# Kernel optimization log

Hardware: AMD Instinct MI355X
Metric: run time of the kernel (lower is better)

The kernel has to match this reference:

```python
import jax, jax.numpy as jnp
import numpy as np

NUM_HEADS = 12


def setup_inputs() -> dict:
    key = jax.random.key(0)
    ks = jax.random.split(key, 5)
    B, S, D = 4, 2048, 768
    scale = 0.02
    return {
        "hidden_states": jax.random.normal(ks[0], (B, S, D), dtype=jnp.float32),
        "c_attn_w": jax.random.normal(ks[1], (D, 3 * D), dtype=jnp.float32) * scale,
        "c_attn_b": jax.random.normal(ks[2], (3 * D,), dtype=jnp.float32) * scale,
        "c_proj_w": jax.random.normal(ks[3], (D, D), dtype=jnp.float32) * scale,
        "c_proj_b": jax.random.normal(ks[4], (D,), dtype=jnp.float32) * scale,
    }


def reference(hidden_states, c_attn_w, c_attn_b, c_proj_w, c_proj_b):
    B, S, D = hidden_states.shape
    H = NUM_HEADS
    hd = D // H

    # fused QKV projection (HF Conv1D: x @ W + b, W is [in, out])
    qkv = hidden_states @ c_attn_w + c_attn_b  # [B, S, 3D]
    q, k, v = jnp.split(qkv, 3, axis=-1)

    def split_heads(t):
        return t.reshape(B, S, H, hd).transpose(0, 2, 1, 3)  # [B, H, S, hd]

    q, k, v = split_heads(q), split_heads(k), split_heads(v)

    # scaled dot-product scores (scale_attn_weights=True -> / sqrt(head_dim))
    scores = jnp.einsum("bhqd,bhkd->bhqk", q, k) / jnp.asarray(
        np.sqrt(hd), dtype=q.dtype
    )

    # causal mask: where(tril, scores, dtype_min) as in eager GPT2Attention
    causal = jnp.tril(jnp.ones((S, S), dtype=bool))
    mask_value = jnp.finfo(scores.dtype).min
    scores = jnp.where(causal[None, None, :, :], scores, mask_value)

    attn = jax.nn.softmax(scores, axis=-1)  # attn_dropout p=0 (eval)

    out = jnp.einsum("bhqk,bhkd->bhqd", attn, v)
    out = out.transpose(0, 2, 1, 3).reshape(B, S, D)  # merge heads

    # output projection (resid_dropout p=0)
    return out @ c_proj_w + c_proj_b
```

## Files before the change

kernel.cpp:

```cpp
#include <hip/hip_runtime.h>
#include <stdint.h>

typedef __attribute__((ext_vector_type(8))) short short8;
typedef __attribute__((ext_vector_type(4))) short short4v;
typedef __attribute__((ext_vector_type(8))) __bf16 bf16x8;
typedef __attribute__((ext_vector_type(4))) float f32x4;

#define SEQ 2048
#define DMODEL 768
#define NHEAD 12
#define HD 64
#define NBATCH 4

__device__ __forceinline__ float bf2f(unsigned short u) {
    return __uint_as_float(((unsigned int)u) << 16);
}
__device__ __forceinline__ unsigned short f2bf(float f) {
    unsigned int u = __float_as_uint(f);
    u += 0x7fffu + ((u >> 16) & 1u);
    return (unsigned short)(u >> 16);
}
__device__ __forceinline__ unsigned short f2bfn(float f) {
    union { __bf16 h; unsigned short u; } cv;
    cv.h = (__bf16)f;
    return cv.u;
}
__device__ __forceinline__ short8 cvt8(float4 a, float4 b) {
    short8 r;
    r[0] = (short)f2bf(a.x); r[1] = (short)f2bf(a.y);
    r[2] = (short)f2bf(a.z); r[3] = (short)f2bf(a.w);
    r[4] = (short)f2bf(b.x); r[5] = (short)f2bf(b.y);
    r[6] = (short)f2bf(b.z); r[7] = (short)f2bf(b.w);
    return r;
}
__device__ __forceinline__ f32x4 mfma16(short8 a, short8 b, f32x4 c) {
    return __builtin_amdgcn_mfma_f32_16x16x32_bf16(
        __builtin_bit_cast(bf16x8, a), __builtin_bit_cast(bf16x8, b), c, 0, 0, 0);
}
__device__ __forceinline__ void gload16(const unsigned short* g, unsigned short* l) {
    __builtin_amdgcn_global_load_lds(
        (const __attribute__((address_space(1))) unsigned int*)g,
        (__attribute__((address_space(3))) unsigned int*)l, 16, 0, 0);
}

__global__ void detect_k(const unsigned short* x, const unsigned short* w1,
                         const unsigned short* b1, const unsigned short* w2,
                         const unsigned short* b2, int* flags) {
    const int w = threadIdx.x >> 6, l = threadIdx.x & 63;
    if (w >= 5) return;
    const unsigned short* ptrs[5] = {x, w1, b1, w2, b2};
    const unsigned short* p = ptrs[w];
    float mx = 0.f;
    for (int j = l; j < 1024; j += 64) {
        float v = fabsf(bf2f(p[j]));
        if (!(v <= 1e30f)) v = 1e31f;
        if (v > mx) mx = v;
    }
#pragma unroll
    for (int off = 1; off < 64; off <<= 1) mx = fmaxf(mx, __shfl_xor(mx, off, 64));
    if (l == 0) flags[w] = (mx > 1e3f) ? 1 : 0;
}

__global__ __launch_bounds__(256) void cvt_x(
    const float* __restrict__ Xf, const unsigned short* __restrict__ Xh,
    unsigned short* __restrict__ Xb, const int* __restrict__ flags, int n8) {
    int i = blockIdx.x * 256 + threadIdx.x;
    if (i >= n8) return;
    if (flags[0]) {
        float4 a = ((const float4*)Xf)[(size_t)i * 2];
        float4 b = ((const float4*)Xf)[(size_t)i * 2 + 1];
        *(short8*)&Xb[(size_t)i * 8] = cvt8(a, b);
    } else {
        ((uint4*)Xb)[i] = ((const uint4*)Xh)[i];
    }
}

__global__ __launch_bounds__(256) void convert_wt(
    const float* __restrict__ Wf, const unsigned short* __restrict__ Wh,
    unsigned short* __restrict__ Wt, int R, int C,
    const int* __restrict__ flags, int fidx) {

    __shared__ unsigned short tile[64][65];
    const int c0 = blockIdx.x * 64, r0 = blockIdx.y * 64;
    const int t = threadIdx.x;
    const int ri = t >> 2, cj = (t & 3) * 16;
    const bool f32 = flags[fidx] != 0;

    if (f32) {
#pragma unroll
        for (int u = 0; u < 4; u++) {
            float4 v = *(const float4*)&Wf[(size_t)(r0 + ri) * C + c0 + cj + u * 4];
            tile[ri][cj + u * 4 + 0] = f2bf(v.x);
            tile[ri][cj + u * 4 + 1] = f2bf(v.y);
            tile[ri][cj + u * 4 + 2] = f2bf(v.z);
            tile[ri][cj + u * 4 + 3] = f2bf(v.w);
        }
    } else {
        uint4 a = *(const uint4*)&Wh[(size_t)(r0 + ri) * C + c0 + cj];
        uint4 b = *(const uint4*)&Wh[(size_t)(r0 + ri) * C + c0 + cj + 8];
        *(uint4*)&tile[ri][cj] = a;
        *(uint4*)&tile[ri][cj + 8] = b;
    }
    __syncthreads();

    const int ci = t >> 2, rj = (t & 3) * 16;
    unsigned short tmp[16];
#pragma unroll
    for (int u = 0; u < 16; u++) tmp[u] = tile[rj + u][ci];
    *(uint4*)&Wt[(size_t)(c0 + ci) * R + r0 + rj]     = *(uint4*)&tmp[0];
    *(uint4*)&Wt[(size_t)(c0 + ci) * R + r0 + rj + 8] = *(uint4*)&tmp[8];
}

__global__ __launch_bounds__(256, 3) void gemm_bt(
    const float* __restrict__ Af, const unsigned short* __restrict__ Ah,
    const unsigned short* __restrict__ Bt,
    const float* __restrict__ biasf, const unsigned short* __restrict__ biash,
    int K, int mode, const int* __restrict__ flags, int aFidx, int bFidx,
    unsigned short* __restrict__ out0, unsigned short* __restrict__ out1,
    unsigned short* __restrict__ out2, float* __restrict__ outf) {

    __shared__ __align__(16) unsigned short As[128][32];
    __shared__ __align__(16) unsigned short Bs[128][32];

    const int mBase = blockIdx.y * 128;
    const int nBase = blockIdx.x * 128;
    const int t = threadIdx.x;
    const int w = t >> 6, l = t & 63, lr = l & 15, lk = l >> 4;
    const int wr = w >> 1, wc = w & 1;

    const bool af32 = (aFidx >= 0) && (flags[aFidx] != 0);
    const bool bf32 = flags[bFidx] != 0;

    f32x4 zero = {0.f, 0.f, 0.f, 0.f};
    f32x4 acc[4][4];
#pragma unroll
    for (int i = 0; i < 4; i++)
#pragma unroll
        for (int j = 0; j < 4; j++) acc[i][j] = zero;

    const int arow = t >> 2;
    const int acol = (t & 3) * 8;
    const float* Afp = Af + (size_t)mBase * K;
    const unsigned short* Ahp = Ah + (size_t)mBase * K;
    const unsigned short* Bp = Bt + (size_t)nBase * K;

    const int ch0 = (w * 2 + 0) * 64 + l;
    const int ch1 = (w * 2 + 1) * 64 + l;
    unsigned short* BsF = &Bs[0][0];
    unsigned short* AsF = &As[0][0];

    for (int k0 = 0; k0 < K; k0 += 32) {
        gload16(&Bp[(size_t)(ch0 >> 2) * K + k0 + (ch0 & 3) * 8], BsF + (size_t)(w * 2 + 0) * 512);
        gload16(&Bp[(size_t)(ch1 >> 2) * K + k0 + (ch1 & 3) * 8], BsF + (size_t)(w * 2 + 1) * 512);
        if (af32) {
            float4 f0 = *(const float4*)&Afp[(size_t)arow * K + k0 + acol];
            float4 f1 = *(const float4*)&Afp[(size_t)arow * K + k0 + acol + 4];
            float4 f2 = *(const float4*)&Afp[(size_t)(arow + 64) * K + k0 + acol];
            float4 f3 = *(const float4*)&Afp[(size_t)(arow + 64) * K + k0 + acol + 4];
            *(short8*)&As[arow][acol]      = cvt8(f0, f1);
            *(short8*)&As[arow + 64][acol] = cvt8(f2, f3);
        } else {
            gload16(&Ahp[(size_t)(ch0 >> 2) * K + k0 + (ch0 & 3) * 8], AsF + (size_t)(w * 2 + 0) * 512);
            gload16(&Ahp[(size_t)(ch1 >> 2) * K + k0 + (ch1 & 3) * 8], AsF + (size_t)(w * 2 + 1) * 512);
        }
        __syncthreads();

        short8 a[4], b[4];
#pragma unroll
        for (int i = 0; i < 4; i++)
            a[i] = *(const short8*)&As[wr * 64 + i * 16 + lr][lk * 8];
#pragma unroll
        for (int j = 0; j < 4; j++)
            b[j] = *(const short8*)&Bs[wc * 64 + j * 16 + lr][lk * 8];
#pragma unroll
        for (int i = 0; i < 4; i++)
#pragma unroll
            for (int j = 0; j < 4; j++) acc[i][j] = mfma16(a[i], b[j], acc[i][j]);
        __syncthreads();
    }

#pragma unroll
    for (int j = 0; j < 4; j++) {
        int col = nBase + wc * 64 + j * 16 + lr;
        float bv = bf32 ? biasf[col] : bf2f(biash[col]);
        if (mode == 0 && col >= 1536) {
            int c2 = col - 1536;
            int h = c2 >> 6, d = c2 & 63;
#pragma unroll
            for (int i = 0; i < 4; i++) {
                int row0 = mBase + wr * 64 + i * 16 + lk * 4;
                int bb = row0 >> 11, s0 = row0 & 2047;
                short4v hv4;
#pragma unroll
                for (int r = 0; r < 4; r++) hv4[r] = (short)f2bf(acc[i][j][r] + bv);
                *(short4v*)&out2[(((size_t)(bb * NHEAD + h)) * HD + d) * SEQ + s0] = hv4;
            }
        } else {
#pragma unroll
            for (int i = 0; i < 4; i++) {
                int row0 = mBase + wr * 64 + i * 16 + lk * 4;
#pragma unroll
                for (int r = 0; r < 4; r++) {
                    int row = row0 + r;
                    float fv = acc[i][j][r] + bv;
                    if (mode == 0) {
                        int bb = row >> 11;
                        int s  = row & 2047;
                        unsigned short hv = f2bf(fv);
                        if (col < 768) {
                            int h = col >> 6, d = col & 63;
                            out0[(((size_t)(bb * NHEAD + h)) * SEQ + s) * HD + d] = hv;
                        } else {
                            int c2 = col - 768;
                            int h = c2 >> 6, d = c2 & 63;
                            out1[(((size_t)(bb * NHEAD + h)) * SEQ + s) * HD + d] = hv;
                        }
                    } else {
                        outf[(size_t)row * DMODEL + col] = fv;
                    }
                }
            }
        }
    }
}

__global__ __launch_bounds__(256, 3) void flash_attn(
    const unsigned short* __restrict__ Q, const unsigned short* __restrict__ Km,
    const unsigned short* __restrict__ Vt, unsigned short* __restrict__ Oatt) {

    const int h  = blockIdx.x;
    const int px = blockIdx.y;
    const int b  = blockIdx.z;
    const int bh = b * NHEAD + h;
    const int qtA = 31 - px;
    const int qtB = px;
    const int t = threadIdx.x, w = t >> 6, l = t & 63, lr = l & 15, lk = l >> 4;
    const int qbA = qtA * 64 + w * 16;
    const int qbB = qtB * 64 + w * 16;

    const unsigned short* Qp = Q + (size_t)bh * SEQ * HD;
    const unsigned short* Kp = Km + (size_t)bh * SEQ * HD;
    const unsigned short* Vp = Vt + (size_t)bh * HD * SEQ;

    __shared__ __align__(16) unsigned short Ks[2][4096];
    __shared__ __align__(16) unsigned short Vs[2][4096];
    __shared__ __align__(16) unsigned short Pb[4][2][1024];

    unsigned short* PwA = &Pb[w][0][0];
    unsigned short* PwB = &Pb[w][1][0];

    short8 qA0 = *(const short8*)&Qp[(size_t)(qbA + lr) * HD + lk * 8];
    short8 qA1 = *(const short8*)&Qp[(size_t)(qbA + lr) * HD + 32 + lk * 8];
    short8 qB0 = *(const short8*)&Qp[(size_t)(qbB + lr) * HD + lk * 8];
    short8 qB1 = *(const short8*)&Qp[(size_t)(qbB + lr) * HD + 32 + lk * 8];

    f32x4 zero = {0.f, 0.f, 0.f, 0.f};
    f32x4 oA[4], oB[4];
    float lA[4] = {0.f, 0.f, 0.f, 0.f}, lB[4] = {0.f, 0.f, 0.f, 0.f};
#pragma unroll
    for (int dt = 0; dt < 4; dt++) { oA[dt] = zero; oB[dt] = zero; }

    const float SCL2E = 0.125f * 1.44269504088896f;

#pragma unroll
    for (int q = 0; q < 2; ++q) {
        const int c = w * 128 + q * 64 + l;
        const int row = c >> 3;
        const int ch = (c & 7) ^ (row & 7);
        gload16(&Kp[(size_t)row * HD + ch * 8], &Ks[0][(w * 128 + q * 64) * 8]);
        gload16(&Vp[(size_t)row * SEQ + ch * 8], &Vs[0][(w * 128 + q * 64) * 8]);
    }
    __syncthreads();

    for (int kt = 0; kt <= qtA; ++kt) {
        const int cur = kt & 1;
        if (kt < qtA) {
            const int kn = kt + 1;
#pragma unroll
            for (int q = 0; q < 2; ++q) {
                const int c = w * 128 + q * 64 + l;
                const int row = c >> 3;
                const int ch = (c & 7) ^ (row & 7);
                gload16(&Kp[(size_t)(kn * 64 + row) * HD + ch * 8],
                        &Ks[cur ^ 1][(w * 128 + q * 64) * 8]);
                gload16(&Vp[(size_t)row * SEQ + kn * 64 + ch * 8],
                        &Vs[cur ^ 1][(w * 128 + q * 64) * 8]);
            }
        }
        const bool doB = (kt <= qtB);

        f32x4 s0[4], s1[4];
#pragma unroll
        for (int ct = 0; ct < 4; ct++) { s0[ct] = zero; s1[ct] = zero; }
#pragma unroll
        for (int ct = 0; ct < 4; ct++) {
            const int row = ct * 16 + lr, sw = row & 7;
            short8 k0 = *(const short8*)&Ks[cur][(row * 8 + (lk ^ sw)) * 8];
            short8 k1 = *(const short8*)&Ks[cur][(row * 8 + ((4 | lk) ^ sw)) * 8];
            s0[ct] = mfma16(qA0, k0, s0[ct]);
            s0[ct] = mfma16(qA1, k1, s0[ct]);
            if (doB) {
                s1[ct] = mfma16(qB0, k0, s1[ct]);
                s1[ct] = mfma16(qB1, k1, s1[ct]);
            }
        }

        {
            float p[4][4];
#pragma unroll
            for (int ct = 0; ct < 4; ct++)
#pragma unroll
                for (int r = 0; r < 4; r++) p[ct][r] = s0[ct][r] * SCL2E;
            if (kt == qtA) {
#pragma unroll
                for (int ct = 0; ct < 4; ct++) {
                    const int col = kt * 64 + ct * 16 + lr;
#pragma unroll
                    for (int r = 0; r < 4; r++)
                        if (col > qbA + lk * 4 + r) p[ct][r] = -30000.0f;
                }
            }
#pragma unroll
            for (int ct = 0; ct < 4; ct++)
#pragma unroll
                for (int r = 0; r < 4; r++) p[ct][r] = exp2f(p[ct][r]);
#pragma unroll
            for (int r = 0; r < 4; r++)
                lA[r] += (p[0][r] + p[1][r]) + (p[2][r] + p[3][r]);
#pragma unroll
            for (int ct = 0; ct < 4; ct++) {
                const int pch = ct * 2 + (lr >> 3);
#pragma unroll
                for (int r = 0; r < 4; r++) {
                    const int prow = lk * 4 + r;
                    PwA[(prow * 8 + (pch ^ (prow & 7))) * 8 + (lr & 7)] = f2bfn(p[ct][r]);
                }
            }
        }
        short8 paA0 = *(const short8*)&PwA[(lr * 8 + (lk ^ (lr & 7))) * 8];
        short8 paA1 = *(const short8*)&PwA[(lr * 8 + ((4 | lk) ^ (lr & 7))) * 8];

        short8 paB0 = {0,0,0,0,0,0,0,0}, paB1 = {0,0,0,0,0,0,0,0};
        if (doB) {
            float p[4][4];
#pragma unroll
            for (int ct = 0; ct < 4; ct++)
#pragma unroll
                for (int r = 0; r < 4; r++) p[ct][r] = s1[ct][r] * SCL2E;
            if (kt == qtB) {
#pragma unroll
                for (int ct = 0; ct < 4; ct++) {
                    const int col = kt * 64 + ct * 16 + lr;
#pragma unroll
                    for (int r = 0; r < 4; r++)
                        if (col > qbB + lk * 4 + r) p[ct][r] = -30000.0f;
                }
            }
#pragma unroll
            for (int ct = 0; ct < 4; ct++)
#pragma unroll
                for (int r = 0; r < 4; r++) p[ct][r] = exp2f(p[ct][r]);
#pragma unroll
            for (int r = 0; r < 4; r++)
                lB[r] += (p[0][r] + p[1][r]) + (p[2][r] + p[3][r]);
#pragma unroll
            for (int ct = 0; ct < 4; ct++) {
                const int pch = ct * 2 + (lr >> 3);
#pragma unroll
                for (int r = 0; r < 4; r++) {
                    const int prow = lk * 4 + r;
                    PwB[(prow * 8 + (pch ^ (prow & 7))) * 8 + (lr & 7)] = f2bfn(p[ct][r]);
                }
            }
            paB0 = *(const short8*)&PwB[(lr * 8 + (lk ^ (lr & 7))) * 8];
            paB1 = *(const short8*)&PwB[(lr * 8 + ((4 | lk) ^ (lr & 7))) * 8];
        }

#pragma unroll
        for (int dt = 0; dt < 4; dt++) {
            const int row = dt * 16 + lr, sw = row & 7;
            short8 v0 = *(const short8*)&Vs[cur][(row * 8 + (lk ^ sw)) * 8];
            short8 v1 = *(const short8*)&Vs[cur][(row * 8 + ((4 | lk) ^ sw)) * 8];
            oA[dt] = mfma16(paA0, v0, oA[dt]);
            oA[dt] = mfma16(paA1, v1, oA[dt]);
            if (doB) {
                oB[dt] = mfma16(paB0, v0, oB[dt]);
                oB[dt] = mfma16(paB1, v1, oB[dt]);
            }
        }
        __syncthreads();
    }

#pragma unroll
    for (int r = 0; r < 4; r++) {
#pragma unroll
        for (int off = 1; off < 16; off <<= 1) {
            lA[r] += __shfl_xor(lA[r], off, 64);
            lB[r] += __shfl_xor(lB[r], off, 64);
        }
    }

#pragma unroll
    for (int r = 0; r < 4; r++) {
        const float invA = 1.0f / lA[r];
        const float invB = 1.0f / lB[r];
        const int rowA = qbA + lk * 4 + r;
        const int rowB = qbB + lk * 4 + r;
#pragma unroll
        for (int dt = 0; dt < 4; dt++) {
            Oatt[((size_t)(b * SEQ) + rowA) * DMODEL + h * HD + dt * 16 + lr] =
                f2bfn(oA[dt][r] * invA);
            Oatt[((size_t)(b * SEQ) + rowB) * DMODEL + h * HD + dt * 16 + lr] =
                f2bfn(oB[dt][r] * invB);
        }
    }
}

extern "C" void kernel_launch(void* const* d_in, const int* in_sizes, int n_in,
                              void* d_out, int out_size, void* d_ws, size_t ws_size,
                              hipStream_t stream) {
    const void *X = d_in[0], *W1 = d_in[1], *b1 = d_in[2], *W2 = d_in[3], *b2 = d_in[4];
    for (int i = 0; i < n_in; i++) {
        switch (in_sizes[i]) {
            case NBATCH * SEQ * DMODEL: X  = d_in[i]; break;
            case DMODEL * 3 * DMODEL:   W1 = d_in[i]; break;
            case 3 * DMODEL:            b1 = d_in[i]; break;
            case DMODEL * DMODEL:       W2 = d_in[i]; break;
            case DMODEL:                b2 = d_in[i]; break;
        }
    }
    float* out = (float*)d_out;

    int* flags = (int*)d_ws;
    unsigned short* base = (unsigned short*)d_ws + 64;
    unsigned short* Wt1 = base;
    unsigned short* Wt2 = Wt1 + (size_t)2304 * 768;

    const size_t headElems = (size_t)NHEAD * SEQ * HD;
    const size_t xElems = (size_t)NBATCH * SEQ * DMODEL;
    const size_t fixedElems = 64 + (size_t)2304 * 768 + (size_t)768 * 768;
    const size_t mergedNeed = (fixedElems + xElems + 4 * NBATCH * headElems) * 2 + 1024;
    const bool merged = ws_size >= mergedNeed;

    detect_k<<<1, 320, 0, stream>>>(
        (const unsigned short*)X, (const unsigned short*)W1,
        (const unsigned short*)b1, (const unsigned short*)W2,
        (const unsigned short*)b2, flags);

    convert_wt<<<dim3(2304 / 64, 768 / 64), 256, 0, stream>>>(
        (const float*)W1, (const unsigned short*)W1, Wt1, 768, 2304, flags, 1);
    convert_wt<<<dim3(768 / 64, 768 / 64), 256, 0, stream>>>(
        (const float*)W2, (const unsigned short*)W2, Wt2, 768, 768, flags, 3);

    if (merged) {
        unsigned short* Xb  = Wt2 + (size_t)768 * 768;
        unsigned short* Qw  = Xb + xElems;
        unsigned short* Kw  = Qw + (size_t)NBATCH * headElems;
        unsigned short* Vtw = Kw + (size_t)NBATCH * headElems;
        unsigned short* Aw  = Vtw + (size_t)NBATCH * headElems;

        cvt_x<<<(int)((xElems / 8 + 255) / 256), 256, 0, stream>>>(
            (const float*)X, (const unsigned short*)X, Xb, flags, (int)(xElems / 8));

        gemm_bt<<<dim3(2304 / 128, NBATCH * SEQ / 128), 256, 0, stream>>>(
            nullptr, Xb, Wt1,
            (const float*)b1, (const unsigned short*)b1,
            DMODEL, 0, flags, -1, 2, Qw, Kw, Vtw, nullptr);

        flash_attn<<<dim3(NHEAD, 16, NBATCH), 256, 0, stream>>>(Qw, Kw, Vtw, Aw);

        gemm_bt<<<dim3(768 / 128, NBATCH * SEQ / 128), 256, 0, stream>>>(
            nullptr, Aw, Wt2,
            (const float*)b2, (const unsigned short*)b2,
            DMODEL, 1, flags, -1, 4, nullptr, nullptr, nullptr, out);
    } else {
        unsigned short* Qw  = Wt2 + (size_t)768 * 768;
        unsigned short* Kw  = Qw + headElems;
        unsigned short* Vtw = Kw + headElems;
        unsigned short* Aw  = Vtw + headElems;
        for (int batch = 0; batch < NBATCH; ++batch) {
            const size_t xoff = (size_t)batch * SEQ * DMODEL;

            gemm_bt<<<dim3(2304 / 128, SEQ / 128), 256, 0, stream>>>(
                (const float*)X + xoff, (const unsigned short*)X + xoff, Wt1,
                (const float*)b1, (const unsigned short*)b1,
                DMODEL, 0, flags, 0, 2, Qw, Kw, Vtw, nullptr);

            flash_attn<<<dim3(NHEAD, 16, 1), 256, 0, stream>>>(Qw, Kw, Vtw, Aw);

            gemm_bt<<<dim3(768 / 128, SEQ / 128), 256, 0, stream>>>(
                nullptr, Aw, Wt2,
                (const float*)b2, (const unsigned short*)b2,
                DMODEL, 1, flags, -1, 4, nullptr, nullptr, nullptr, out + xoff);
        }
    }
}
```

Baseline: 249.8 us.

## Keep softmax probabilities in registers via transposed QK^T and add XCD-aware GEMM swizzle

Attention now computes S^T by swapping the MFMA operand order, so each lane's output fragment directly forms the A operand of 16x16x16 bf16 MFMAs for the PV product. This removes the per-wave LDS round-trip for P and shrinks the row-sum reductions. V fragments are reread as 4-element chunks. The GEMM also remaps block IDs so neighbouring tiles land on the same XCD for better L2 reuse. The cost is twice as many smaller-K MFMA instructions for PV and more V registers.

After: 241.8 us. -3.2%, faster.

```diff
diff --git a/kernel.cpp b/kernel.cpp
--- a/kernel.cpp
+++ b/kernel.cpp
@@ -36,6 +36,14 @@
 __device__ __forceinline__ f32x4 mfma16(short8 a, short8 b, f32x4 c) {
     return __builtin_amdgcn_mfma_f32_16x16x32_bf16(
         __builtin_bit_cast(bf16x8, a), __builtin_bit_cast(bf16x8, b), c, 0, 0, 0);
+}
+__device__ __forceinline__ f32x4 mfma16k16(short4v a, short4v b, f32x4 c) {
+#if __has_builtin(__builtin_amdgcn_mfma_f32_16x16x16bf16_1k)
+    return __builtin_amdgcn_mfma_f32_16x16x16bf16_1k(a, b, c, 0, 0, 0);
+#else
+    asm("v_mfma_f32_16x16x16_bf16 %0, %1, %2, %0" : "+v"(c) : "v"(a), "v"(b));
+    return c;
+#endif
 }
 __device__ __forceinline__ void gload16(const unsigned short* g, unsigned short* l) {
     __builtin_amdgcn_global_load_lds(
@@ -122,8 +130,19 @@
     __shared__ __align__(16) unsigned short As[128][32];
     __shared__ __align__(16) unsigned short Bs[128][32];
 
-    const int mBase = blockIdx.y * 128;
-    const int nBase = blockIdx.x * 128;
+    int bx = blockIdx.x, by = blockIdx.y;
+    {
+        const int nwg = (int)(gridDim.x * gridDim.y);
+        if ((nwg & 7) == 0) {
+            int bid = by * gridDim.x + bx;
+            const int cpx = nwg >> 3;
+            bid = (bid & 7) * cpx + (bid >> 3);
+            bx = bid % gridDim.x;
+            by = bid / gridDim.x;
+        }
+    }
+    const int mBase = by * 128;
+    const int nBase = bx * 128;
     const int t = threadIdx.x;
     const int w = t >> 6, l = t & 63, lr = l & 15, lk = l >> 4;
     const int wr = w >> 1, wc = w & 1;
@@ -244,10 +263,6 @@
 
     __shared__ __align__(16) unsigned short Ks[2][4096];
     __shared__ __align__(16) unsigned short Vs[2][4096];
-    __shared__ __align__(16) unsigned short Pb[4][2][1024];
-
-    unsigned short* PwA = &Pb[w][0][0];
-    unsigned short* PwB = &Pb[w][1][0];
 
     short8 qA0 = *(const short8*)&Qp[(size_t)(qbA + lr) * HD + lk * 8];
     short8 qA1 = *(const short8*)&Qp[(size_t)(qbA + lr) * HD + 32 + lk * 8];
@@ -256,7 +271,7 @@
 
     f32x4 zero = {0.f, 0.f, 0.f, 0.f};
     f32x4 oA[4], oB[4];
-    float lA[4] = {0.f, 0.f, 0.f, 0.f}, lB[4] = {0.f, 0.f, 0.f, 0.f};
+    float lsumA = 0.f, lsumB = 0.f;
 #pragma unroll
     for (int dt = 0; dt < 4; dt++) { oA[dt] = zero; oB[dt] = zero; }
 
@@ -297,14 +312,28 @@
             const int row = ct * 16 + lr, sw = row & 7;
             short8 k0 = *(const short8*)&Ks[cur][(row * 8 + (lk ^ sw)) * 8];
             short8 k1 = *(const short8*)&Ks[cur][(row * 8 + ((4 | lk) ^ sw)) * 8];
-            s0[ct] = mfma16(qA0, k0, s0[ct]);
-            s0[ct] = mfma16(qA1, k1, s0[ct]);
+            s0[ct] = mfma16(k0, qA0, s0[ct]);
+            s0[ct] = mfma16(k1, qA1, s0[ct]);
             if (doB) {
-                s1[ct] = mfma16(qB0, k0, s1[ct]);
-                s1[ct] = mfma16(qB1, k1, s1[ct]);
-            }
-        }
-
+                s1[ct] = mfma16(k0, qB0, s1[ct]);
+                s1[ct] = mfma16(k1, qB1, s1[ct]);
+            }
+        }
+
+        short4v vf[4][4];
+#pragma unroll
+        for (int dt = 0; dt < 4; dt++) {
+            const int row = dt * 16 + lr;
+            const int sw = row & 7;
+#pragma unroll
+            for (int ct = 0; ct < 4; ct++) {
+                const int g = 2 * ct + (lk >> 1);
+                const int hh = lk & 1;
+                vf[dt][ct] = *(const short4v*)&Vs[cur][(row * 8 + (g ^ sw)) * 8 + hh * 4];
+            }
+        }
+
+        short4v paA[4];
         {
             float p[4][4];
 #pragma unroll
@@ -312,12 +341,14 @@
 #pragma unroll
                 for (int r = 0; r < 4; r++) p[ct][r] = s0[ct][r] * SCL2E;
             if (kt == qtA) {
+                const int qrow = qbA + lr;
 #pragma unroll
                 for (int ct = 0; ct < 4; ct++) {
-                    const int col = kt * 64 + ct * 16 + lr;
-#pragma unroll
-                    for (int r = 0; r < 4; r++)
-                        if (col > qbA + lk * 4 + r) p[ct][r] = -30000.0f;
+#pragma unroll
+                    for (int r = 0; r < 4; r++) {
+                        const int key = kt * 64 + ct * 16 + lk * 4 + r;
+                        if (key > qrow) p[ct][r] = -30000.0f;
+                    }
                 }
             }
 #pragma unroll
@@ -325,35 +356,38 @@
 #pragma unroll
                 for (int r = 0; r < 4; r++) p[ct][r] = exp2f(p[ct][r]);
 #pragma unroll
-            for (int r = 0; r < 4; r++)
-                lA[r] += (p[0][r] + p[1][r]) + (p[2][r] + p[3][r]);
+            for (int ct = 0; ct < 4; ct++)
+                lsumA += (p[ct][0] + p[ct][1]) + (p[ct][2] + p[ct][3]);
 #pragma unroll
             for (int ct = 0; ct < 4; ct++) {
-                const int pch = ct * 2 + (lr >> 3);
-#pragma unroll
-                for (int r = 0; r < 4; r++) {
-                    const int prow = lk * 4 + r;
-                    PwA[(prow * 8 + (pch ^ (prow & 7))) * 8 + (lr & 7)] = f2bfn(p[ct][r]);
-                }
-            }
-        }
-        short8 paA0 = *(const short8*)&PwA[(lr * 8 + (lk ^ (lr & 7))) * 8];
-        short8 paA1 = *(const short8*)&PwA[(lr * 8 + ((4 | lk) ^ (lr & 7))) * 8];
-
-        short8 paB0 = {0,0,0,0,0,0,0,0}, paB1 = {0,0,0,0,0,0,0,0};
+                short4v pk;
+#pragma unroll
+                for (int r = 0; r < 4; r++) pk[r] = (short)f2bfn(p[ct][r]);
+                paA[ct] = pk;
+            }
+        }
+#pragma unroll
+        for (int dt = 0; dt < 4; dt++)
+#pragma unroll
+            for (int ct = 0; ct < 4; ct++)
+                oA[dt] = mfma16k16(paA[ct], vf[dt][ct], oA[dt]);
+
         if (doB) {
+            short4v paB[4];
             float p[4][4];
 #pragma unroll
             for (int ct = 0; ct < 4; ct++)
 #pragma unroll
                 for (int r = 0; r < 4; r++) p[ct][r] = s1[ct][r] * SCL2E;
             if (kt == qtB) {
+                const int qrow = qbB + lr;
 #pragma unroll
                 for (int ct = 0; ct < 4; ct++) {
-                    const int col = kt * 64 + ct * 16 + lr;
-#pragma unroll
-                    for (int r = 0; r < 4; r++)
-                        if (col > qbB + lk * 4 + r) p[ct][r] = -30000.0f;
+#pragma unroll
+                    for (int r = 0; r < 4; r++) {
+                        const int key = kt * 64 + ct * 16 + lk * 4 + r;
+                        if (key > qrow) p[ct][r] = -30000.0f;
+                    }
                 }
             }
 #pragma unroll
@@ -361,49 +395,34 @@
 #pragma unroll
                 for (int r = 0; r < 4; r++) p[ct][r] = exp2f(p[ct][r]);
 #pragma unroll
-            for (int r = 0; r < 4; r++)
-                lB[r] += (p[0][r] + p[1][r]) + (p[2][r] + p[3][r]);
+            for (int ct = 0; ct < 4; ct++)
+                lsumB += (p[ct][0] + p[ct][1]) + (p[ct][2] + p[ct][3]);
 #pragma unroll
             for (int ct = 0; ct < 4; ct++) {
-                const int pch = ct * 2 + (lr >> 3);
-#pragma unroll
-                for (int r = 0; r < 4; r++) {
-                    const int prow = lk * 4 + r;
-                    PwB[(prow * 8 + (pch ^ (prow & 7))) * 8 + (lr & 7)] = f2bfn(p[ct][r]);
-                }
-            }
-            paB0 = *(const short8*)&PwB[(lr * 8 + (lk ^ (lr & 7))) * 8];
-            paB1 = *(const short8*)&PwB[(lr * 8 + ((4 | lk) ^ (lr & 7))) * 8];
-        }
-
-#pragma unroll
-        for (int dt = 0; dt < 4; dt++) {
-            const int row = dt * 16 + lr, sw = row & 7;
-            short8 v0 = *(const short8*)&Vs[cur][(row * 8 + (lk ^ sw)) * 8];
-            short8 v1 = *(const short8*)&Vs[cur][(row * 8 + ((4 | lk) ^ sw)) * 8];
-            oA[dt] = mfma16(paA0, v0, oA[dt]);
-            oA[dt] = mfma16(paA1, v1, oA[dt]);
-            if (doB) {
-                oB[dt] = mfma16(paB0, v0, oB[dt]);
-                oB[dt] = mfma16(paB1, v1, oB[dt]);
-            }
-        }
+                short4v pk;
+#pragma unroll
+                for (int r = 0; r < 4; r++) pk[r] = (short)f2bfn(p[ct][r]);
+                paB[ct] = pk;
+            }
+#pragma unroll
+            for (int dt = 0; dt < 4; dt++)
+#pragma unroll
+                for (int ct = 0; ct < 4; ct++)
+                    oB[dt] = mfma16k16(paB[ct], vf[dt][ct], oB[dt]);
+        }
+
         __syncthreads();
     }
 
+    lsumA += __shfl_xor(lsumA, 16, 64);
+    lsumA += __shfl_xor(lsumA, 32, 64);
+    lsumB += __shfl_xor(lsumB, 16, 64);
+    lsumB += __shfl_xor(lsumB, 32, 64);
+
 #pragma unroll
     for (int r = 0; r < 4; r++) {
-#pragma unroll
-        for (int off = 1; off < 16; off <<= 1) {
-            lA[r] += __shfl_xor(lA[r], off, 64);
-            lB[r] += __shfl_xor(lB[r], off, 64);
-        }
-    }
-
-#pragma unroll
-    for (int r = 0; r < 4; r++) {
-        const float invA = 1.0f / lA[r];
-        const float invB = 1.0f / lB[r];
+        const float invA = 1.0f / __shfl(lsumA, lk * 4 + r, 64);
+        const float invB = 1.0f / __shfl(lsumB, lk * 4 + r, 64);
         const int rowA = qbA + lk * 4 + r;
         const int rowB = qbB + lk * 4 + r;
 #pragma unroll
```
